# Kernel tuning notes

Hardware: AMD Instinct MI355X
Metric: run time of the kernel (lower is better)

The kernel has to match this reference:

```python
import jax, jax.numpy as jnp
import numpy as np

B, S, D = 64, 512, 768   # batch, seq_len, bert hidden
H = D // 2               # per-direction LSTM hidden (384)
T = 9                    # tag_num
L, NDIR = 2, 2           # lstm layers, directions


def setup_inputs() -> dict:
    key = jax.random.key(0)
    ks = jax.random.split(key, 10)
    def n(k, shape, s=0.05):
        return jax.random.normal(k, shape, jnp.float32) * s
    return {
        "bert_output": jax.random.normal(ks[0], (B, S, D), jnp.float32),
        "y": jax.random.randint(ks[1], (B, S), 0, T),
        "lstm_Wih": n(ks[2], (L, NDIR, 4 * H, D)),   # input_size==D for both layers (bi-output = D)
        "lstm_Whh": n(ks[3], (L, NDIR, 4 * H, H)),
        "lstm_b":   n(ks[4], (L, NDIR, 4 * H)),      # b_ih + b_hh fused (mathematically identical)
        "fc_w": n(ks[5], (T, D)),
        "fc_b": n(ks[6], (T,)),
        "trans":   n(ks[7], (T, T), 0.1),
        "start_t": n(ks[8], (T,), 0.1),
        "end_t":   n(ks[9], (T,), 0.1),
    }


def _lstm_dir(x, Wih, Whh, b):
    # x: [B,S,I] -> [B,S,H]; PyTorch gate order i,f,g,o
    Bq, Hq = x.shape[0], Whh.shape[1]
    def step(carry, xt):
        h, c = carry
        g = xt @ Wih.T + h @ Whh.T + b          # [B,4H]
        i, f, gg, o = jnp.split(g, 4, axis=-1)
        c = jax.nn.sigmoid(f) * c + jax.nn.sigmoid(i) * jnp.tanh(gg)
        h = jax.nn.sigmoid(o) * jnp.tanh(c)
        return (h, c), h
    z = jnp.zeros((Bq, Hq), x.dtype)
    _, hs = jax.lax.scan(step, (z, z), jnp.swapaxes(x, 0, 1))
    return jnp.swapaxes(hs, 0, 1)


def _bilstm(x, Wih, Whh, b):
    for l in range(L):
        fwd = _lstm_dir(x, Wih[l, 0], Whh[l, 0], b[l, 0])
        bwd = jnp.flip(_lstm_dir(jnp.flip(x, 1), Wih[l, 1], Whh[l, 1], b[l, 1]), 1)
        x = jnp.concatenate([fwd, bwd], axis=-1)  # [B,S,2H]=[B,S,D]
    return x


def _crf_nll(em, tags, trans, start_t, end_t):
    # em: [B,S,T] emissions; tags: [B,S] int. Negative mean log-likelihood.
    gold = (
        jnp.take_along_axis(em, tags[..., None], axis=-1)[..., 0].sum(-1)
        + trans[tags[:, :-1], tags[:, 1:]].sum(-1)
        + start_t[tags[:, 0]] + end_t[tags[:, -1]]
    )  # [B]
    def step(alpha, em_t):  # alpha,em_t: [B,T]
        a = jax.nn.logsumexp(alpha[:, :, None] + trans[None], axis=1) + em_t
        return a, None
    alpha0 = start_t[None] + em[:, 0]
    alpha, _ = jax.lax.scan(step, alpha0, jnp.swapaxes(em[:, 1:], 0, 1))
    logZ = jax.nn.logsumexp(alpha + end_t[None], axis=-1)  # [B]
    return jnp.mean(logZ - gold)


def _viterbi(em, trans, start_t, end_t):
    def step(v, em_t):
        scores = v[:, :, None] + trans[None]      # [B,Tprev,Tcur]
        bp = jnp.argmax(scores, axis=1)           # [B,T]
        return jnp.max(scores, axis=1) + em_t, bp
    v0 = start_t[None] + em[:, 0]
    v, bps = jax.lax.scan(step, v0, jnp.swapaxes(em[:, 1:], 0, 1))  # bps: [S-1,B,T]
    last = jnp.argmax(v + end_t[None], axis=-1)   # [B]
    def back(tag, bp):
        prev = jnp.take_along_axis(bp, tag[:, None], axis=1)[:, 0]
        return prev, tag
    first, rest = jax.lax.scan(back, last, bps, reverse=True)  # rest: tags at 1..S-1
    tags = jnp.concatenate([first[None], rest], axis=0)        # [S,B]
    return jnp.swapaxes(tags, 0, 1)               # [B,S]


def reference(bert_output, y, lstm_Wih, lstm_Whh, lstm_b, fc_w, fc_b, trans, start_t, end_t):
    h = _bilstm(bert_output, lstm_Wih, lstm_Whh, lstm_b)
    em = h @ fc_w.T + fc_b                        # [B,S,T]
    loss = _crf_nll(em, y, trans, start_t, end_t)
    tag = _viterbi(em, trans, start_t, end_t)
    return (loss, tag)
```

## Files before the change

kernel.cpp:

```cpp
#include <hip/hip_runtime.h>

#define Bn   64
#define Sn   512
#define Dn   768
#define Hn   384
#define G4n  1536
#define Tn   9
#define SCHn 128
#define NCH  4

#define OFF_WIHB  0ull
#define SZ_WIHB   (2ull * Dn * G4n)
#define OFF_GATES (OFF_WIHB + SZ_WIHB)
#define SZ_GATES  (2ull * Bn * SCHn * G4n)
#define OFF_H1B   (OFF_GATES + SZ_GATES)
#define SZ_H1B    ((unsigned long long)Bn * Sn * Dn / 2)
#define OFF_BERTB (OFF_H1B + SZ_H1B)
#define SZ_BERTB  ((unsigned long long)Bn * Sn * Dn / 2)
#define OFF_EMP   (OFF_BERTB + SZ_BERTB)
#define SZ_EMP    (2ull * Bn * Sn * Tn)
#define OFF_EM    (OFF_EMP + SZ_EMP)
#define SZ_EM     ((unsigned long long)Bn * Sn * Tn)
#define OFF_HBUF  (OFF_EM + SZ_EM)
#define SZ_HBUF   (2ull * 2 * Bn * Hn)
#define OFF_CST   (OFF_HBUF + SZ_HBUF)
#define SZ_CST    (2ull * Bn * Hn)
#define OFF_LP    (OFF_CST + SZ_CST)
#define SZ_LP     64ull
#define OFF_STAMP (OFF_LP + SZ_LP)
#define STAMP_TOTAL (2 * 8 * 32 * 32)

typedef __attribute__((ext_vector_type(8))) short short8v;
typedef __attribute__((ext_vector_type(8))) unsigned short ushort8v;
typedef __attribute__((ext_vector_type(4))) float f32x4;

static __device__ __forceinline__ float sigf(float x) { return 1.f / (1.f + expf(-x)); }

static __device__ __forceinline__ unsigned short f2bf(float x) {
    unsigned u = __float_as_uint(x);
    u += 0x7fffu + ((u >> 16) & 1u);
    return (unsigned short)(u >> 16);
}

static __device__ __forceinline__ unsigned long long llc_load_u64(const unsigned long long* p) {
    return __hip_atomic_load(p, __ATOMIC_RELAXED, __HIP_MEMORY_SCOPE_SYSTEM);
}
static __device__ __forceinline__ void llc_store_f32(float* p, float v) {
    __hip_atomic_store(p, v, __ATOMIC_RELAXED, __HIP_MEMORY_SCOPE_SYSTEM);
}
static __device__ __forceinline__ int llc_load_i32(const int* p) {
    return __hip_atomic_load(p, __ATOMIC_RELAXED, __HIP_MEMORY_SCOPE_SYSTEM);
}

__global__ void to_bf16(const float* __restrict__ in, unsigned short* __restrict__ out,
                        int total)
{
    for (int i = blockIdx.x * 256 + threadIdx.x; i < total; i += gridDim.x * 256)
        out[i] = f2bf(in[i]);
}

__global__ void init_bar(int* __restrict__ st)
{
    const int i = blockIdx.x * 256 + threadIdx.x;
    if (i < STAMP_TOTAL) st[i] = 0;
}

__global__ __launch_bounds__(256) void gemm_gates(
    const unsigned short* __restrict__ Abf,
    const unsigned short* __restrict__ Wb,
    const float* __restrict__ bvec,
    float* __restrict__ G,
    int layer, int chunk)
{
    const int tid = threadIdx.x;
    const int nb  = blockIdx.x;
    const int mb  = blockIdx.y;
    const int m0  = mb * 128;
    const int dir = mb >> 6;
    const int n0c = nb * 128;

    __shared__ unsigned short As[128][40];
    __shared__ unsigned short Bs[128][40];

    const unsigned short* BT = Wb + (size_t)(layer * 2 + dir) * G4n * Dn;
    const float* bias = bvec + (size_t)(layer * 2 + dir) * G4n;

    const int mm   = tid >> 1;
    const int seg  = (tid & 1) * 16;
    const int rem  = (m0 + mm) & 8191;
    const int bb   = rem >> 7;
    const int j    = rem & 127;
    const int p    = chunk * SCHn + j;
    const int s    = dir ? (Sn - 1 - p) : p;
    const unsigned short* arow = Abf + ((size_t)bb * Sn + s) * Dn;
    const unsigned short* brow = BT + (size_t)(n0c + mm) * Dn;

    const int l = tid & 63, wave = tid >> 6;
    const int wy = wave >> 1, wx = wave & 1;
    const int fr = l & 15, fk = (l >> 4) * 8;

    f32x4 acc[4][4];
    #pragma unroll
    for (int mt = 0; mt < 4; ++mt)
        #pragma unroll
        for (int nt = 0; nt < 4; ++nt)
            acc[mt][nt] = (f32x4){0.f, 0.f, 0.f, 0.f};

    for (int k0 = 0; k0 < Dn; k0 += 32) {
        const ushort8v a0 = *(const ushort8v*)(arow + k0 + seg);
        const ushort8v a1 = *(const ushort8v*)(arow + k0 + seg + 8);
        const ushort8v b0 = *(const ushort8v*)(brow + k0 + seg);
        const ushort8v b1 = *(const ushort8v*)(brow + k0 + seg + 8);
        __syncthreads();
        *(ushort8v*)&As[mm][seg]     = a0;
        *(ushort8v*)&As[mm][seg + 8] = a1;
        *(ushort8v*)&Bs[mm][seg]     = b0;
        *(ushort8v*)&Bs[mm][seg + 8] = b1;
        __syncthreads();

        short8v af[4], bf[4];
        #pragma unroll
        for (int mt = 0; mt < 4; ++mt)
            af[mt] = *(const short8v*)&As[wy * 64 + mt * 16 + fr][fk];
        #pragma unroll
        for (int nt = 0; nt < 4; ++nt)
            bf[nt] = *(const short8v*)&Bs[wx * 64 + nt * 16 + fr][fk];
        #pragma unroll
        for (int mt = 0; mt < 4; ++mt)
            #pragma unroll
            for (int nt = 0; nt < 4; ++nt)
                acc[mt][nt] = __builtin_amdgcn_mfma_f32_16x16x32_bf16(
                    af[mt], bf[nt], acc[mt][nt], 0, 0, 0);
    }

    #pragma unroll
    for (int nt = 0; nt < 4; ++nt) {
        const int n  = n0c + wx * 64 + nt * 16 + fr;
        const int g  = n / 384;
        const int d2 = n - g * 384;
        const int gcol = d2 * 4 + g;
        const float bv = bias[n];
        #pragma unroll
        for (int mt = 0; mt < 4; ++mt) {
            #pragma unroll
            for (int q = 0; q < 4; ++q) {
                const int row = m0 + wy * 64 + mt * 16 + (l >> 4) * 4 + q;
                G[(size_t)row * G4n + gcol] = acc[mt][nt][q] + bv;
            }
        }
    }
}

__global__ __launch_bounds__(256, 2) void lstm_persist(
    const float* __restrict__ gates,
    const float* __restrict__ Whh,
    const float* __restrict__ fcw,
    unsigned short* __restrict__ h1b,
    float* __restrict__ emP,
    float* __restrict__ hbuf,
    float* __restrict__ cst,
    int* __restrict__ stamps,
    int layer, int chunk)
{
    const int tid = threadIdx.x;
    const int bid = blockIdx.x;
    const int dir = bid >> 8;
    const int bg  = (bid >> 5) & 7;
    const int dg  = bid & 31;
    const int b0 = bg * 8, d0 = dg * 12;

    __shared__ __align__(16) float hstage[8][396];
    __shared__ __align__(16) float red[4][16][28];
    __shared__ float cs[8][12];
    __shared__ float fcwl[Hn];

    const int ct = tid & 15;
    const int kq = tid >> 4;
    const int k0 = kq * 24;
    const int sbb = tid >> 5, skq = tid & 31;
    const bool pw = (tid < 96);
    const int pb = tid / 12, pdd = tid - pb * 12;
    const int lane = tid & 63, wv = tid >> 6;

    float wreg[72];
    {
        const float* Wbase = Whh + (size_t)(layer * 2 + dir) * G4n * Hn;
        #pragma unroll
        for (int c = 0; c < 3; ++c) {
            const int cc = ct * 3 + c;
            const int dd = cc >> 2, g = cc & 3;
            const float* wr = Wbase + (size_t)(g * Hn + d0 + dd) * Hn + k0;
            #pragma unroll
            for (int kk = 0; kk < 24; kk += 4) {
                const float4 w4 = *(const float4*)(wr + kk);
                wreg[c * 24 + kk + 0] = w4.x;
                wreg[c * 24 + kk + 1] = w4.y;
                wreg[c * 24 + kk + 2] = w4.z;
                wreg[c * 24 + kk + 3] = w4.w;
            }
        }
    }

    const bool fcwg = (layer == 1) && (dg < Tn);
    if (fcwg) {
        for (int k2 = tid; k2 < Hn; k2 += 256)
            fcwl[k2] = fcw[dg * Dn + dir * Hn + k2];
    }

    if (pw) {
        cs[pb][pdd] = (chunk == 0) ? 0.f
            : cst[((size_t)dir * Bn + b0 + pb) * Hn + d0 + pdd];
    }
    __syncthreads();

    const int* mystamps = stamps + ((dir * 8 + bg) * 32 + skq) * 32;

    for (int j = 0; j < SCHn; ++j) {
        const int sg = chunk * SCHn + j;
        const int p_rd = sg & 1, p_wr = (sg + 1) & 1;
        const int s = dir ? (Sn - 1 - sg) : sg;

        float4 g4 = make_float4(0.f, 0.f, 0.f, 0.f);
        if (pw)
            g4 = *(const float4*)(gates +
                  (((size_t)(dir * Bn + b0 + pb) * SCHn + j) * G4n) + (d0 + pdd) * 4);

        if (chunk == 0 && j == 0) {
            #pragma unroll
            for (int i = 0; i < 6; ++i)
                *(float2*)&hstage[sbb][skq * 12 + 2 * i] = make_float2(0.f, 0.f);
        } else {
            const int need = layer * Sn + sg;
            while (llc_load_i32(mystamps) < need) __builtin_amdgcn_s_sleep(1);
            const unsigned long long* hsrc = (const unsigned long long*)
                (hbuf + ((size_t)(p_rd * 2 + dir) * Bn + b0 + sbb) * Hn) + skq * 6;
            #pragma unroll
            for (int i = 0; i < 6; ++i) {
                const unsigned long long v = llc_load_u64(hsrc + i);
                float2 f2;
                f2.x = __uint_as_float((unsigned int)v);
                f2.y = __uint_as_float((unsigned int)(v >> 32));
                *(float2*)&hstage[sbb][skq * 12 + 2 * i] = f2;
            }
        }
        __syncthreads();

        float acc[24];
        #pragma unroll
        for (int i = 0; i < 24; ++i) acc[i] = 0.f;
        #pragma unroll
        for (int b = 0; b < 8; ++b) {
            const float* hp = &hstage[b][k0];
            float hv[24];
            #pragma unroll
            for (int i = 0; i < 6; ++i) {
                const float4 h4 = *(const float4*)(hp + i * 4);
                hv[i * 4 + 0] = h4.x; hv[i * 4 + 1] = h4.y;
                hv[i * 4 + 2] = h4.z; hv[i * 4 + 3] = h4.w;
            }
            #pragma unroll
            for (int c = 0; c < 3; ++c)
                #pragma unroll
                for (int kk = 0; kk < 24; ++kk)
                    acc[b * 3 + c] += hv[kk] * wreg[c * 24 + kk];
        }
        #pragma unroll
        for (int i = 0; i < 24; ++i) {
            acc[i] += __shfl_xor(acc[i], 16);
            acc[i] += __shfl_xor(acc[i], 32);
        }
        if (lane < 16) {
            #pragma unroll
            for (int i = 0; i < 24; i += 4) {
                float4 t4; t4.x = acc[i]; t4.y = acc[i + 1];
                t4.z = acc[i + 2]; t4.w = acc[i + 3];
                *(float4*)&red[wv][lane][i] = t4;
            }
        }

        if (fcwg && j >= 1) {
            const int sgp = sg - 1;
            const int sprev = dir ? (Sn - 1 - sgp) : sgp;
            const float* hp2 = &hstage[sbb][skq * 12];
            const float* wp2 = &fcwl[skq * 12];
            float e2 = 0.f;
            #pragma unroll
            for (int q = 0; q < 12; ++q) e2 += hp2[q] * wp2[q];
            e2 += __shfl_down(e2, 16, 32);
            e2 += __shfl_down(e2, 8, 32);
            e2 += __shfl_down(e2, 4, 32);
            e2 += __shfl_down(e2, 2, 32);
            e2 += __shfl_down(e2, 1, 32);
            if (skq == 0)
                emP[((size_t)(dir * Bn + b0 + sbb) * Sn + sprev) * Tn + dg] = e2;
        }
        __syncthreads();

        if (pw) {
            float pre[4];
            #pragma unroll
            for (int g = 0; g < 4; ++g) {
                const int cc = pdd * 4 + g;
                const int ct2 = cc / 3;
                const int e = pb * 3 + (cc - ct2 * 3);
                pre[g] = red[0][ct2][e] + red[1][ct2][e]
                       + red[2][ct2][e] + red[3][ct2][e];
            }
            const float ii = sigf(pre[0] + g4.x);
            const float ff = sigf(pre[1] + g4.y);
            const float gg = tanhf(pre[2] + g4.z);
            const float oo = sigf(pre[3] + g4.w);
            const float cn = ff * cs[pb][pdd] + ii * gg;
            cs[pb][pdd] = cn;
            const float hn = oo * tanhf(cn);
            llc_store_f32(&hbuf[((size_t)(p_wr * 2 + dir) * Bn + b0 + pb) * Hn + d0 + pdd], hn);
            if (layer == 0)
                h1b[((size_t)(b0 + pb) * Sn + s) * Dn + dir * Hn + d0 + pdd] = f2bf(hn);
        }
        __syncthreads();
        if (tid == 0)
            __hip_atomic_store(stamps + ((dir * 8 + bg) * 32 + dg) * 32,
                               layer * Sn + sg + 1, __ATOMIC_RELAXED,
                               __HIP_MEMORY_SCOPE_SYSTEM);
    }

    if (fcwg) {
        const int sgl = chunk * SCHn + SCHn - 1;
        const int need = layer * Sn + sgl + 1;
        while (llc_load_i32(mystamps) < need) __builtin_amdgcn_s_sleep(1);
        const int pp = (sgl + 1) & 1;
        const unsigned long long* hsrc = (const unsigned long long*)
            (hbuf + ((size_t)(pp * 2 + dir) * Bn + b0 + sbb) * Hn) + skq * 6;
        #pragma unroll
        for (int i = 0; i < 6; ++i) {
            const unsigned long long v = llc_load_u64(hsrc + i);
            float2 f2;
            f2.x = __uint_as_float((unsigned int)v);
            f2.y = __uint_as_float((unsigned int)(v >> 32));
            *(float2*)&hstage[sbb][skq * 12 + 2 * i] = f2;
        }
        __syncthreads();
        const int sprev = dir ? (Sn - 1 - sgl) : sgl;
        const float* hp2 = &hstage[sbb][skq * 12];
        const float* wp2 = &fcwl[skq * 12];
        float e2 = 0.f;
        #pragma unroll
        for (int q = 0; q < 12; ++q) e2 += hp2[q] * wp2[q];
        e2 += __shfl_down(e2, 16, 32);
        e2 += __shfl_down(e2, 8, 32);
        e2 += __shfl_down(e2, 4, 32);
        e2 += __shfl_down(e2, 2, 32);
        e2 += __shfl_down(e2, 1, 32);
        if (skq == 0)
            emP[((size_t)(dir * Bn + b0 + sbb) * Sn + sprev) * Tn + dg] = e2;
    }

    if (pw)
        cst[((size_t)dir * Bn + b0 + pb) * Hn + d0 + pdd] = cs[pb][pdd];
}

__global__ void em_combine(const float* __restrict__ emP, const float* __restrict__ fcb,
                           float* __restrict__ em)
{
    const int idx = blockIdx.x * 256 + threadIdx.x;
    if (idx < Bn * Sn * Tn) {
        const int t = idx % Tn;
        em[idx] = emP[idx] + emP[(size_t)Bn * Sn * Tn + idx] + fcb[t];
    }
}

__global__ __launch_bounds__(64) void crf_loss(
    const float* __restrict__ em, const int* __restrict__ y,
    const float* __restrict__ trans, const float* __restrict__ start_t,
    const float* __restrict__ end_t, float* __restrict__ lossp)
{
    const int b = blockIdx.x, tid = threadIdx.x;
    __shared__ float tr[Tn * Tn];
    for (int i = tid; i < Tn * Tn; i += 64) tr[i] = trans[i];
    __syncthreads();
    const int* yb = y + (size_t)b * Sn;
    const float* emb = em + (size_t)b * Sn * Tn;

    float gs = 0.f;
    for (int s2 = tid; s2 < Sn; s2 += 64) gs += emb[s2 * Tn + yb[s2]];
    for (int s2 = tid; s2 < Sn - 1; s2 += 64) gs += tr[yb[s2] * Tn + yb[s2 + 1]];
    #pragma unroll
    for (int o = 32; o > 0; o >>= 1) gs += __shfl_down(gs, o, 64);

    const int jj = (tid < Tn) ? tid : 0;
    float alpha = start_t[jj] + emb[jj];
    for (int s2 = 1; s2 < Sn; ++s2) {
        float av[Tn];
        #pragma unroll
        for (int i = 0; i < Tn; ++i) av[i] = __shfl(alpha, i, 64) + tr[i * Tn + jj];
        float m = av[0];
        #pragma unroll
        for (int i = 1; i < Tn; ++i) m = fmaxf(m, av[i]);
        float ss = 0.f;
        #pragma unroll
        for (int i = 0; i < Tn; ++i) ss += expf(av[i] - m);
        alpha = logf(ss) + m + emb[s2 * Tn + jj];
    }
    const float xv = alpha + end_t[jj];
    float m9 = -1e30f, vv[Tn];
    #pragma unroll
    for (int i = 0; i < Tn; ++i) { vv[i] = __shfl(xv, i, 64); m9 = fmaxf(m9, vv[i]); }
    float s9 = 0.f;
    #pragma unroll
    for (int i = 0; i < Tn; ++i) s9 += expf(vv[i] - m9);
    const float logZ = logf(s9) + m9;
    if (tid == 0) lossp[b] = logZ - (gs + start_t[yb[0]] + end_t[yb[Sn - 1]]);
}

__global__ __launch_bounds__(64) void loss_final(const float* __restrict__ lossp,
                                                 float* __restrict__ out)
{
    float v = lossp[threadIdx.x];
    #pragma unroll
    for (int o = 32; o > 0; o >>= 1) v += __shfl_down(v, o, 64);
    if (threadIdx.x == 0) out[0] = v * (1.f / 64.f);
}

__global__ __launch_bounds__(64) void viterbi_k(
    const float* __restrict__ em, const float* __restrict__ trans,
    const float* __restrict__ start_t, const float* __restrict__ end_t,
    float* __restrict__ out)
{
    const int b = blockIdx.x, tid = threadIdx.x;
    __shared__ float tr[Tn * Tn];
    __shared__ unsigned char bp[Sn - 1][16];
    __shared__ float vfin[Tn];
    for (int i = tid; i < Tn * Tn; i += 64) tr[i] = trans[i];
    __syncthreads();
    const float* emb = em + (size_t)b * Sn * Tn;
    const int jj = (tid < Tn) ? tid : 0;
    float v = start_t[jj] + emb[jj];
    for (int s2 = 1; s2 < Sn; ++s2) {
        float vv[Tn];
        #pragma unroll
        for (int i = 0; i < Tn; ++i) vv[i] = __shfl(v, i, 64);
        float best = -1e30f; int bi = 0;
        #pragma unroll
        for (int i = 0; i < Tn; ++i) {
            const float sc = vv[i] + tr[i * Tn + jj];
            if (sc > best) { best = sc; bi = i; }
        }
        if (tid < Tn) bp[s2 - 1][tid] = (unsigned char)bi;
        v = best + emb[s2 * Tn + jj];
    }
    if (tid < Tn) vfin[tid] = v + end_t[tid];
    __syncthreads();
    if (tid == 0) {
        float best = -1e30f; int cur = 0;
        for (int i = 0; i < Tn; ++i) if (vfin[i] > best) { best = vfin[i]; cur = i; }
        float* ob = out + 1 + (size_t)b * Sn;
        ob[Sn - 1] = (float)cur;
        for (int s2 = Sn - 1; s2 >= 1; --s2) { cur = bp[s2 - 1][cur]; ob[s2 - 1] = (float)cur; }
    }
}

extern "C" void kernel_launch(void* const* d_in, const int* in_sizes, int n_in,
                              void* d_out, int out_size, void* d_ws, size_t ws_size,
                              hipStream_t stream)
{
    (void)in_sizes; (void)n_in; (void)out_size; (void)ws_size;
    const float* bert  = (const float*)d_in[0];
    const int*   y     = (const int*)d_in[1];
    const float* Wih   = (const float*)d_in[2];
    const float* Whh   = (const float*)d_in[3];
    const float* bvec  = (const float*)d_in[4];
    const float* fcw   = (const float*)d_in[5];
    const float* fcb   = (const float*)d_in[6];
    const float* trans = (const float*)d_in[7];
    const float* stt   = (const float*)d_in[8];
    const float* ent   = (const float*)d_in[9];
    float* out = (float*)d_out;
    float* ws  = (float*)d_ws;

    unsigned short* Wihb  = (unsigned short*)(ws + OFF_WIHB);
    float* gates = ws + OFF_GATES;
    unsigned short* h1b   = (unsigned short*)(ws + OFF_H1B);
    unsigned short* bertb = (unsigned short*)(ws + OFF_BERTB);
    float* emP   = ws + OFF_EMP;
    float* em    = ws + OFF_EM;
    float* hbuf  = ws + OFF_HBUF;
    float* cst   = ws + OFF_CST;
    float* lossp = ws + OFF_LP;
    int*   stamps = (int*)(ws + OFF_STAMP);

    init_bar<<<dim3((STAMP_TOTAL + 255) / 256), dim3(256), 0, stream>>>(stamps);
    to_bf16<<<dim3(2048), dim3(256), 0, stream>>>(Wih, Wihb, 4 * G4n * Dn);
    to_bf16<<<dim3(2048), dim3(256), 0, stream>>>(bert, bertb, Bn * Sn * Dn);

    for (int l = 0; l < 2; ++l) {
        const unsigned short* A = (l == 0) ? bertb : h1b;
        for (int c = 0; c < NCH; ++c) {
            gemm_gates<<<dim3(12, 128), dim3(256), 0, stream>>>(A, Wihb, bvec, gates, l, c);
            lstm_persist<<<dim3(512), dim3(256), 0, stream>>>(gates, Whh, fcw, h1b, emP,
                                                              hbuf, cst, stamps, l, c);
        }
    }

    em_combine<<<dim3((Bn * Sn * Tn + 255) / 256), dim3(256), 0, stream>>>(emP, fcb, em);
    crf_loss<<<dim3(Bn), dim3(64), 0, stream>>>(em, y, trans, stt, ent, lossp);
    loss_final<<<dim3(1), dim3(64), 0, stream>>>(lossp, out);
    viterbi_k<<<dim3(Bn), dim3(64), 0, stream>>>(em, trans, stt, ent, out);
}
```

Baseline: 9.271 ms.

## Overlap next-chunk gate GEMM with LSTM recurrence and store gates in bf16

The persistent LSTM kernel now launches 2048 blocks. Blocks 0-511 run the recurrence for the current chunk, and the extra blocks compute the input-gate GEMM for the next chunk into a double-buffered gate workspace. This hides the GEMM behind the latency-bound recurrence instead of running it serially between launches. The gate pre-activations are also stored as bf16 to halve the traffic of writing and reading them. The per-step barrier is replaced by per-wave stamp writes after a vmcnt wait, and readers poll both wave stamps with one 64-bit load. The risks are extra rounding error in the gates, GEMM blocks competing with the spinning persistent blocks for CU resources, and co-residency assumptions in the spin-wait scheme.

```diff
diff --git a/kernel.cpp b/kernel.cpp
--- a/kernel.cpp
+++ b/kernel.cpp
@@ -11,9 +11,10 @@
 
 #define OFF_WIHB  0ull
 #define SZ_WIHB   (2ull * Dn * G4n)
-#define OFF_GATES (OFF_WIHB + SZ_WIHB)
-#define SZ_GATES  (2ull * Bn * SCHn * G4n)
-#define OFF_H1B   (OFF_GATES + SZ_GATES)
+#define OFF_GATESB (OFF_WIHB + SZ_WIHB)
+#define SGATE_U16 (2ull * Bn * SCHn * G4n)
+#define SZ_GATESB (SGATE_U16)
+#define OFF_H1B   (OFF_GATESB + SZ_GATESB)
 #define SZ_H1B    ((unsigned long long)Bn * Sn * Dn / 2)
 #define OFF_BERTB (OFF_H1B + SZ_H1B)
 #define SZ_BERTB  ((unsigned long long)Bn * Sn * Dn / 2)
@@ -31,7 +32,6 @@
 #define STAMP_TOTAL (2 * 8 * 32 * 32)
 
 typedef __attribute__((ext_vector_type(8))) short short8v;
-typedef __attribute__((ext_vector_type(8))) unsigned short ushort8v;
 typedef __attribute__((ext_vector_type(4))) float f32x4;
 
 static __device__ __forceinline__ float sigf(float x) { return 1.f / (1.f + expf(-x)); }
@@ -41,6 +41,9 @@
     u += 0x7fffu + ((u >> 16) & 1u);
     return (unsigned short)(u >> 16);
 }
+static __device__ __forceinline__ float bf2f(unsigned short u) {
+    return __uint_as_float(((unsigned)u) << 16);
+}
 
 static __device__ __forceinline__ unsigned long long llc_load_u64(const unsigned long long* p) {
     return __hip_atomic_load(p, __ATOMIC_RELAXED, __HIP_MEMORY_SCOPE_SYSTEM);
@@ -48,9 +51,6 @@
 static __device__ __forceinline__ void llc_store_f32(float* p, float v) {
     __hip_atomic_store(p, v, __ATOMIC_RELAXED, __HIP_MEMORY_SCOPE_SYSTEM);
 }
-static __device__ __forceinline__ int llc_load_i32(const int* p) {
-    return __hip_atomic_load(p, __ATOMIC_RELAXED, __HIP_MEMORY_SCOPE_SYSTEM);
-}
 
 __global__ void to_bf16(const float* __restrict__ in, unsigned short* __restrict__ out,
                         int total)
@@ -65,22 +65,17 @@
     if (i < STAMP_TOTAL) st[i] = 0;
 }
 
-__global__ __launch_bounds__(256) void gemm_gates(
+static __device__ __forceinline__ void gemm_tile(
+    unsigned short As[][40], unsigned short Bs[][40],
     const unsigned short* __restrict__ Abf,
     const unsigned short* __restrict__ Wb,
     const float* __restrict__ bvec,
-    float* __restrict__ G,
-    int layer, int chunk)
-{
-    const int tid = threadIdx.x;
-    const int nb  = blockIdx.x;
-    const int mb  = blockIdx.y;
+    unsigned short* __restrict__ G,
+    int layer, int chunk, int nb, int mb, int tid)
+{
     const int m0  = mb * 128;
     const int dir = mb >> 6;
     const int n0c = nb * 128;
-
-    __shared__ unsigned short As[128][40];
-    __shared__ unsigned short Bs[128][40];
 
     const unsigned short* BT = Wb + (size_t)(layer * 2 + dir) * G4n * Dn;
     const float* bias = bvec + (size_t)(layer * 2 + dir) * G4n;
@@ -107,15 +102,15 @@
             acc[mt][nt] = (f32x4){0.f, 0.f, 0.f, 0.f};
 
     for (int k0 = 0; k0 < Dn; k0 += 32) {
-        const ushort8v a0 = *(const ushort8v*)(arow + k0 + seg);
-        const ushort8v a1 = *(const ushort8v*)(arow + k0 + seg + 8);
-        const ushort8v b0 = *(const ushort8v*)(brow + k0 + seg);
-        const ushort8v b1 = *(const ushort8v*)(brow + k0 + seg + 8);
+        const short8v a0 = *(const short8v*)(arow + k0 + seg);
+        const short8v a1 = *(const short8v*)(arow + k0 + seg + 8);
+        const short8v b0 = *(const short8v*)(brow + k0 + seg);
+        const short8v b1 = *(const short8v*)(brow + k0 + seg + 8);
         __syncthreads();
-        *(ushort8v*)&As[mm][seg]     = a0;
-        *(ushort8v*)&As[mm][seg + 8] = a1;
-        *(ushort8v*)&Bs[mm][seg]     = b0;
-        *(ushort8v*)&Bs[mm][seg + 8] = b1;
+        *(short8v*)&As[mm][seg]     = a0;
+        *(short8v*)&As[mm][seg + 8] = a1;
+        *(short8v*)&Bs[mm][seg]     = b0;
+        *(short8v*)&Bs[mm][seg + 8] = b1;
         __syncthreads();
 
         short8v af[4], bf[4];
@@ -145,14 +140,26 @@
             #pragma unroll
             for (int q = 0; q < 4; ++q) {
                 const int row = m0 + wy * 64 + mt * 16 + (l >> 4) * 4 + q;
-                G[(size_t)row * G4n + gcol] = acc[mt][nt][q] + bv;
-            }
-        }
-    }
-}
-
-__global__ __launch_bounds__(256, 2) void lstm_persist(
-    const float* __restrict__ gates,
+                G[(size_t)row * G4n + gcol] = f2bf(acc[mt][nt][q] + bv);
+            }
+        }
+    }
+}
+
+__global__ __launch_bounds__(256) void gemm_gates(
+    const unsigned short* __restrict__ Abf,
+    const unsigned short* __restrict__ Wb,
+    const float* __restrict__ bvec,
+    unsigned short* __restrict__ G,
+    int layer, int chunk)
+{
+    __shared__ __align__(16) unsigned short As[128][40];
+    __shared__ __align__(16) unsigned short Bs[128][40];
+    gemm_tile(As, Bs, Abf, Wb, bvec, G, layer, chunk, blockIdx.x, blockIdx.y, threadIdx.x);
+}
+
+__global__ __launch_bounds__(256, 2) void lstm_fused(
+    const unsigned short* __restrict__ grd,
     const float* __restrict__ Whh,
     const float* __restrict__ fcw,
     unsigned short* __restrict__ h1b,
@@ -160,19 +167,35 @@
     float* __restrict__ hbuf,
     float* __restrict__ cst,
     int* __restrict__ stamps,
-    int layer, int chunk)
-{
+    int layer, int chunk,
+    const unsigned short* __restrict__ gA,
+    const unsigned short* __restrict__ Wb,
+    const float* __restrict__ bvec,
+    unsigned short* __restrict__ gwr,
+    int glayer, int gchunk, int gvalid)
+{
+    __shared__ __align__(16) float smemf[5440];
     const int tid = threadIdx.x;
     const int bid = blockIdx.x;
+
+    if (bid >= 512) {
+        if (!gvalid) return;
+        const int gb = bid - 512;
+        gemm_tile((unsigned short(*)[40])smemf,
+                  (unsigned short(*)[40])(smemf + 2560),
+                  gA, Wb, bvec, gwr, glayer, gchunk, gb % 12, gb / 12, tid);
+        return;
+    }
+
+    float (*hstage)[396]  = (float(*)[396])smemf;
+    float (*red)[16][28]  = (float(*)[16][28])(smemf + 3168);
+    float (*cs)[12]       = (float(*)[12])(smemf + 4960);
+    float* fcwl           = smemf + 5056;
+
     const int dir = bid >> 8;
     const int bg  = (bid >> 5) & 7;
     const int dg  = bid & 31;
     const int b0 = bg * 8, d0 = dg * 12;
-
-    __shared__ __align__(16) float hstage[8][396];
-    __shared__ __align__(16) float red[4][16][28];
-    __shared__ float cs[8][12];
-    __shared__ float fcwl[Hn];
 
     const int ct = tid & 15;
     const int kq = tid >> 4;
@@ -182,6 +205,10 @@
     const int pb = tid / 12, pdd = tid - pb * 12;
     const int lane = tid & 63, wv = tid >> 6;
 
+    int* sgrp = stamps + ((dir * 8 + bg) * 32) * 32;
+    const unsigned long long* pollp =
+        (const unsigned long long*)(sgrp + skq * 32);
+
     float wreg[72];
     {
         const float* Wbase = Whh + (size_t)(layer * 2 + dir) * G4n * Hn;
@@ -213,17 +240,18 @@
     }
     __syncthreads();
 
-    const int* mystamps = stamps + ((dir * 8 + bg) * 32 + skq) * 32;
-
     for (int j = 0; j < SCHn; ++j) {
         const int sg = chunk * SCHn + j;
         const int p_rd = sg & 1, p_wr = (sg + 1) & 1;
         const int s = dir ? (Sn - 1 - sg) : sg;
 
         float4 g4 = make_float4(0.f, 0.f, 0.f, 0.f);
-        if (pw)
-            g4 = *(const float4*)(gates +
+        if (pw) {
+            const ushort4 gu = *(const ushort4*)(grd +
                   (((size_t)(dir * Bn + b0 + pb) * SCHn + j) * G4n) + (d0 + pdd) * 4);
+            g4.x = bf2f(gu.x); g4.y = bf2f(gu.y);
+            g4.z = bf2f(gu.z); g4.w = bf2f(gu.w);
+        }
 
         if (chunk == 0 && j == 0) {
             #pragma unroll
@@ -231,7 +259,11 @@
                 *(float2*)&hstage[sbb][skq * 12 + 2 * i] = make_float2(0.f, 0.f);
         } else {
             const int need = layer * Sn + sg;
-            while (llc_load_i32(mystamps) < need) __builtin_amdgcn_s_sleep(1);
+            unsigned long long sv = llc_load_u64(pollp);
+            while ((int)(unsigned)sv < need || (int)(sv >> 32) < need) {
+                __builtin_amdgcn_s_sleep(1);
+                sv = llc_load_u64(pollp);
+            }
             const unsigned long long* hsrc = (const unsigned long long*)
                 (hbuf + ((size_t)(p_rd * 2 + dir) * Bn + b0 + sbb) * Hn) + skq * 6;
             #pragma unroll
@@ -317,17 +349,23 @@
             if (layer == 0)
                 h1b[((size_t)(b0 + pb) * Sn + s) * Dn + dir * Hn + d0 + pdd] = f2bf(hn);
         }
-        __syncthreads();
-        if (tid == 0)
-            __hip_atomic_store(stamps + ((dir * 8 + bg) * 32 + dg) * 32,
-                               layer * Sn + sg + 1, __ATOMIC_RELAXED,
-                               __HIP_MEMORY_SCOPE_SYSTEM);
+        if (tid < 128) {
+            asm volatile("s_waitcnt vmcnt(0)" ::: "memory");
+            if ((tid & 63) == 0)
+                __hip_atomic_store(sgrp + dg * 32 + (tid >> 6),
+                                   layer * Sn + sg + 1,
+                                   __ATOMIC_RELAXED, __HIP_MEMORY_SCOPE_SYSTEM);
+        }
     }
 
     if (fcwg) {
         const int sgl = chunk * SCHn + SCHn - 1;
         const int need = layer * Sn + sgl + 1;
-        while (llc_load_i32(mystamps) < need) __builtin_amdgcn_s_sleep(1);
+        unsigned long long sv = llc_load_u64(pollp);
+        while ((int)(unsigned)sv < need || (int)(sv >> 32) < need) {
+            __builtin_amdgcn_s_sleep(1);
+            sv = llc_load_u64(pollp);
+        }
         const int pp = (sgl + 1) & 1;
         const unsigned long long* hsrc = (const unsigned long long*)
             (hbuf + ((size_t)(pp * 2 + dir) * Bn + b0 + sbb) * Hn) + skq * 6;
@@ -478,7 +516,7 @@
     float* ws  = (float*)d_ws;
 
     unsigned short* Wihb  = (unsigned short*)(ws + OFF_WIHB);
-    float* gates = ws + OFF_GATES;
+    unsigned short* gatesb = (unsigned short*)(ws + OFF_GATESB);
     unsigned short* h1b   = (unsigned short*)(ws + OFF_H1B);
     unsigned short* bertb = (unsigned short*)(ws + OFF_BERTB);
     float* emP   = ws + OFF_EMP;
@@ -492,13 +530,18 @@
     to_bf16<<<dim3(2048), dim3(256), 0, stream>>>(Wih, Wihb, 4 * G4n * Dn);
     to_bf16<<<dim3(2048), dim3(256), 0, stream>>>(bert, bertb, Bn * Sn * Dn);
 
-    for (int l = 0; l < 2; ++l) {
+    gemm_gates<<<dim3(12, 128), dim3(256), 0, stream>>>(bertb, Wihb, bvec, gatesb, 0, 0);
+    for (int k = 0; k < 8; ++k) {
+        const int l = k >> 2, c = k & 3;
+        const int gv = (c < 3) ? 1 : 0;
         const unsigned short* A = (l == 0) ? bertb : h1b;
-        for (int c = 0; c < NCH; ++c) {
-            gemm_gates<<<dim3(12, 128), dim3(256), 0, stream>>>(A, Wihb, bvec, gates, l, c);
-            lstm_persist<<<dim3(512), dim3(256), 0, stream>>>(gates, Whh, fcw, h1b, emP,
-                                                              hbuf, cst, stamps, l, c);
-        }
+        lstm_fused<<<dim3(2048), dim3(256), 0, stream>>>(
+            gatesb + (size_t)(c & 1) * SGATE_U16, Whh, fcw, h1b, emP, hbuf, cst, stamps,
+            l, c,
+            A, Wihb, bvec, gatesb + (size_t)((c + 1) & 1) * SGATE_U16, l, c + 1, gv);
+        if (k == 3)
+            gemm_gates<<<dim3(12, 128), dim3(256), 0, stream>>>(h1b, Wihb, bvec,
+                                                                gatesb, 1, 0);
     }
 
     em_combine<<<dim3((Bn * Sn * Tn + 255) / 256), dim3(256), 0, stream>>>(emP, fcb, em);
```

New measurement: 11.29 ms. 1.22x slower.
